# Performance work log

Measured on AMD Instinct MI355X. Metric: run time of the kernel, lower is better.

## Reference

```python
import jax, jax.numpy as jnp
import numpy as np

C = 128          # num_channels
HID = 256        # mlp hidden = 2*C
HEAD_DIM = 16    # C // num_heads (8)
SCALE = 1.0 / np.sqrt(HEAD_DIM)
EPS = 1e-5


def _linear_init(key, fan_in, fan_out):
    kw, kb = jax.random.split(key)
    s = 1.0 / np.sqrt(fan_in)
    w = jax.random.uniform(kw, (fan_in, fan_out), minval=-s, maxval=s, dtype=jnp.float32)
    b = jax.random.uniform(kb, (fan_out,), minval=-s, maxval=s, dtype=jnp.float32)
    return w, b


def setup_inputs() -> dict:
    key = jax.random.key(0)
    ks = jax.random.split(key, 8)
    x = jax.random.normal(ks[0], (4, C, 64, 64), dtype=jnp.float32)
    wq, bq = _linear_init(ks[1], C, C)
    wk, bk = _linear_init(ks[2], C, C)
    wv, bv = _linear_init(ks[3], C, C)
    wo, bo = _linear_init(ks[4], C, C)
    w1, b1 = _linear_init(ks[5], C, HID)
    w2, b2 = _linear_init(ks[6], HID, C)
    return {
        "x": x,
        "ln1_w": jnp.ones((C,), jnp.float32), "ln1_b": jnp.zeros((C,), jnp.float32),
        "wq": wq, "bq": bq, "wk": wk, "bk": bk, "wv": wv, "bv": bv,
        "wo": wo, "bo": bo,
        "ln2_w": jnp.ones((C,), jnp.float32), "ln2_b": jnp.zeros((C,), jnp.float32),
        "w1": w1, "b1": b1, "w2": w2, "b2": b2,
    }


def _layernorm(x, w, b):
    mu = jnp.mean(x, axis=-1, keepdims=True)
    var = jnp.mean(jnp.square(x - mu), axis=-1, keepdims=True)
    return (x - mu) * jax.lax.rsqrt(var + EPS) * w + b


def reference(x, ln1_w, ln1_b, wq, bq, wk, bk, wv, bv, wo, bo, ln2_w, ln2_b, w1, b1, w2, b2):
    B, Cc, H, W = x.shape
    t = x.reshape(B, Cc, H * W).transpose(0, 2, 1)  # [B, S, C]
    xl = _layernorm(t, ln1_w, ln1_b)
    q = xl @ wq + bq
    k = xl @ wk + bk
    v = xl @ wv + bv
    scores = jnp.einsum('bqc,bkc->bqk', q, k) * SCALE  # [B, S, S]
    # Faithful to source: softmax over dim=1 (the QUERY axis).
    attn = jax.nn.softmax(scores, axis=1)
    att_out = jnp.einsum('bqk,bkc->bqc', attn, v) @ wo + bo
    t = att_out + t
    m = _layernorm(t, ln2_w, ln2_b) @ w1 + b1
    m = jax.nn.gelu(m, approximate=False) @ w2 + b2
    t = jax.nn.gelu(m, approximate=False) + t  # second GELU per source
    return t.transpose(0, 2, 1).reshape(B, Cc, H, W)
```

## Files before the change

kernel.cpp:

```cpp
#include <hip/hip_runtime.h>
#include <math.h>

#define S 4096
#define CNUM 128
#define BATCH 4
#define MTOT (BATCH * S)
#define SCLOG2E 0.36067376022224085f
#define EPSLN 1e-5f
#define KSPLIT 8
#define QSPLIT 8


typedef __attribute__((ext_vector_type(8))) short bf16x8;
typedef __attribute__((ext_vector_type(4))) float f32x4;
typedef __attribute__((ext_vector_type(16))) float f32x16;
typedef __attribute__((ext_vector_type(4))) unsigned int u32x4;

__device__ __forceinline__ float gelu_exact(float x) {
    return 0.5f * x * (1.0f + erff(x * 0.7071067811865476f));
}

__device__ __forceinline__ unsigned short f2b(float f) {
    union { float f; unsigned int u; } v; v.f = f;
    unsigned int r = (v.u + 0x7FFFu + ((v.u >> 16) & 1u)) >> 16;
    return (unsigned short)r;
}
__device__ __forceinline__ float b2f(unsigned short u) {
    return __uint_as_float((unsigned)u << 16);
}
__device__ __forceinline__ int swz(int col, int row) {
    return ((((col >> 3) ^ (row & 15)) << 3) | (col & 7));
}

__device__ __forceinline__ void gl_lds16(const void* g, void* l) {
    __builtin_amdgcn_global_load_lds(
        (__attribute__((address_space(1))) void*)g,
        (__attribute__((address_space(3))) void*)l, 16, 0, 0);
}

__global__ __launch_bounds__(256) void ln1_transpose(
    const float* __restrict__ x, const float* __restrict__ w, const float* __restrict__ bb,
    unsigned short* __restrict__ xlh, float* __restrict__ t)
{
    __shared__ float tile[128][65];
    __shared__ float mu[64], rs[64];
    const int b = blockIdx.y;
    const int s0 = blockIdx.x * 64;
    const float* xb = x + (size_t)b * CNUM * S;
    for (int i = threadIdx.x; i < 128 * 64; i += 256) {
        int c = i >> 6, sl = i & 63;
        tile[c][sl] = xb[(size_t)c * S + s0 + sl];
    }
    __syncthreads();
    if (threadIdx.x < 64) {
        float sum = 0.f, sq = 0.f;
        for (int c = 0; c < 128; ++c) {
            float v = tile[c][threadIdx.x];
            sum += v; sq += v * v;
        }
        float m = sum * (1.f / 128.f);
        float var = sq * (1.f / 128.f) - m * m;
        mu[threadIdx.x] = m;
        rs[threadIdx.x] = rsqrtf(var + EPSLN);
    }
    __syncthreads();
    for (int i = threadIdx.x; i < 128 * 64; i += 256) {
        int c = i & 127, sl = i >> 7;
        float v = tile[c][sl];
        size_t row = (size_t)b * S + s0 + sl;
        t[row * CNUM + c] = v;
        xlh[row * CNUM + swz(c, sl)] = f2b((v - mu[sl]) * rs[sl] * w[c] + bb[c]);
    }
}

__global__ __launch_bounds__(256) void convw(
    const float* __restrict__ wq, const float* __restrict__ wk, const float* __restrict__ wv,
    const float* __restrict__ wo, const float* __restrict__ w1, const float* __restrict__ w2,
    const float* __restrict__ bq, const float* __restrict__ bk, const float* __restrict__ bv,
    unsigned short* __restrict__ wqkvh, unsigned short* __restrict__ woh,
    unsigned short* __restrict__ w1h, unsigned short* __restrict__ w2h,
    float* __restrict__ bqkv)
{
    int a = blockIdx.y;
    int idx = blockIdx.x * 256 + threadIdx.x;
    if (a == 6) {
        if (idx < 128) bqkv[idx] = bq[idx];
        else if (idx < 256) bqkv[idx] = bk[idx - 128];
        else if (idx < 384) bqkv[idx] = bv[idx - 256];
        return;
    }
    const float* src; unsigned short* dst; int Nsh, Ksz;
    switch (a) {
        case 0: src = wq; dst = wqkvh;          Nsh = 7; Ksz = 128; break;
        case 1: src = wk; dst = wqkvh + 16384;  Nsh = 7; Ksz = 128; break;
        case 2: src = wv; dst = wqkvh + 32768;  Nsh = 7; Ksz = 128; break;
        case 3: src = wo; dst = woh;            Nsh = 7; Ksz = 128; break;
        case 4: src = w1; dst = w1h;            Nsh = 8; Ksz = 128; break;
        default: src = w2; dst = w2h;           Nsh = 7; Ksz = 256; break;
    }
    int total = Ksz << Nsh;
    if (idx >= total) return;
    int k = idx >> Nsh, n = idx & ((1 << Nsh) - 1);
    dst[n * Ksz + swz(k, n)] = f2b(src[idx]);
}

template<int KT, int EPI>
__global__ __launch_bounds__(256) void gemm_mfma(
    const unsigned short* __restrict__ A, const unsigned short* __restrict__ Bt,
    const float* __restrict__ bias, const float* __restrict__ res,
    void* __restrict__ Cv, void* __restrict__ Cv2,
    const float* __restrict__ wln, const float* __restrict__ bln, int N)
{
    constexpr int CH = KT / 8;
    constexpr int CSH = (KT == 128) ? 4 : 5;
    __shared__ unsigned short As[64 * KT];
    __shared__ unsigned short Bs[128 * KT];
    __shared__ float2 lnred[2][64];
    const int bm = blockIdx.y * 64;
    const int bn = blockIdx.x * 128;
    const int z = blockIdx.z;
    const unsigned short* Btz = (EPI == 7) ? Bt + z * 16384 : Bt;
    const float* biasz = (EPI == 7) ? bias + z * 128 : bias;
    const int tid = threadIdx.x;
    const int w = tid >> 6, l = tid & 63;
    const int rw = (w & 1) * 32, cw = (w >> 1) * 64;
    const int lm = l & 15, lq = l >> 4;

    if (EPI == 3) {
        #pragma unroll
        for (int i = 0; i < (64 * CH) / 256; ++i) {
            int cid = i * 256 + tid;
            int r = cid >> CSH, c = cid & (CH - 1);
            int p = (c & ~15) | ((c ^ r) & 15);
            float s8[8];
            #pragma unroll
            for (int j = 0; j < 8; ++j) s8[j] = 0.f;
            #pragma unroll
            for (int pp = 0; pp < KSPLIT; ++pp) {
                const unsigned short* src = A + (size_t)pp * ((size_t)MTOT * CNUM)
                                              + (size_t)(bm + r) * KT + c * 8;
                ushort4 u0 = *(const ushort4*)(src);
                ushort4 u1 = *(const ushort4*)(src + 4);
                s8[0] += b2f(u0.x); s8[1] += b2f(u0.y); s8[2] += b2f(u0.z); s8[3] += b2f(u0.w);
                s8[4] += b2f(u1.x); s8[5] += b2f(u1.y); s8[6] += b2f(u1.z); s8[7] += b2f(u1.w);
            }
            ushort4 o0, o1;
            o0.x = f2b(s8[0]); o0.y = f2b(s8[1]); o0.z = f2b(s8[2]); o0.w = f2b(s8[3]);
            o1.x = f2b(s8[4]); o1.y = f2b(s8[5]); o1.z = f2b(s8[6]); o1.w = f2b(s8[7]);
            *(ushort4*)(As + r * KT + p * 8) = o0;
            *(ushort4*)(As + r * KT + p * 8 + 4) = o1;
        }
    } else {
        #pragma unroll
        for (int i = 0; i < KT / 32; ++i)
            gl_lds16(A + (size_t)bm * KT + (i * 256 + tid) * 8, As + (i * 256 + tid) * 8);
    }
    #pragma unroll
    for (int i = 0; i < KT / 16; ++i)
        gl_lds16(Btz + (size_t)bn * KT + (i * 256 + tid) * 8, Bs + (i * 256 + tid) * 8);
    __syncthreads();

    f32x4 zero = {0.f, 0.f, 0.f, 0.f};
    f32x4 acc[2][4];
    #pragma unroll
    for (int i = 0; i < 2; ++i)
        #pragma unroll
        for (int j = 0; j < 4; ++j) acc[i][j] = zero;

    #pragma unroll
    for (int ks = 0; ks < KT / 32; ++ks) {
        int c_lin = ks * 4 + lq;
        bf16x8 a[2], bfr[4];
        #pragma unroll
        for (int i = 0; i < 2; ++i) {
            int m = rw + i * 16 + lm;
            int p = (c_lin & ~15) | ((c_lin ^ m) & 15);
            a[i] = *(const bf16x8*)(As + m * KT + p * 8);
        }
        #pragma unroll
        for (int j = 0; j < 4; ++j) {
            int n = cw + j * 16 + lm;
            int p = (c_lin & ~15) | ((c_lin ^ n) & 15);
            bfr[j] = *(const bf16x8*)(Bs + n * KT + p * 8);
        }
        #pragma unroll
        for (int i = 0; i < 2; ++i)
            #pragma unroll
            for (int j = 0; j < 4; ++j)
                acc[i][j] = __builtin_amdgcn_mfma_f32_16x16x32_bf16(a[i], bfr[j], acc[i][j], 0, 0, 0);
    }

    if (EPI == 3) {
        float vv[2][4][4];
        #pragma unroll
        for (int i = 0; i < 2; ++i) {
            int rowbase = bm + rw + i * 16 + lq * 4;
            #pragma unroll
            for (int j = 0; j < 4; ++j) {
                int col = bn + cw + j * 16 + lm;
                #pragma unroll
                for (int reg = 0; reg < 4; ++reg)
                    vv[i][j][reg] = acc[i][j][reg] + biasz[col] +
                                    res[(size_t)(rowbase + reg) * N + col];
            }
        }
        #pragma unroll
        for (int i = 0; i < 2; ++i)
            #pragma unroll
            for (int reg = 0; reg < 4; ++reg) {
                float s = 0.f, q = 0.f;
                #pragma unroll
                for (int j = 0; j < 4; ++j) {
                    float xv = vv[i][j][reg];
                    s += xv; q += xv * xv;
                }
                #pragma unroll
                for (int off = 1; off < 16; off <<= 1) {
                    s += __shfl_xor(s, off);
                    q += __shfl_xor(q, off);
                }
                if (lm == 0) {
                    float2 sq2; sq2.x = s; sq2.y = q;
                    lnred[cw >> 6][rw + i * 16 + lq * 4 + reg] = sq2;
                }
            }
        __syncthreads();
        #pragma unroll
        for (int i = 0; i < 2; ++i) {
            #pragma unroll
            for (int reg = 0; reg < 4; ++reg) {
                int lrow = rw + i * 16 + lq * 4 + reg;
                int row = bm + lrow;
                float2 h0 = lnred[0][lrow], h1 = lnred[1][lrow];
                float mean = (h0.x + h1.x) * (1.f / 128.f);
                float var  = (h0.y + h1.y) * (1.f / 128.f) - mean * mean;
                float rs = rsqrtf(var + EPSLN);
                #pragma unroll
                for (int j = 0; j < 4; ++j) {
                    int col = bn + cw + j * 16 + lm;
                    float xv = vv[i][j][reg];
                    ((float*)Cv)[(size_t)row * N + col] = xv;
                    ((unsigned short*)Cv2)[(size_t)row * N + swz(col, lrow)] =
                        f2b((xv - mean) * rs * wln[col] + bln[col]);
                }
            }
        }
        return;
    }

    #pragma unroll
    for (int i = 0; i < 2; ++i) {
        int rowbase = bm + rw + i * 16 + lq * 4;
        #pragma unroll
        for (int j = 0; j < 4; ++j) {
            int col = bn + cw + j * 16 + lm;
            float v[4];
            #pragma unroll
            for (int reg = 0; reg < 4; ++reg) v[reg] = acc[i][j][reg] + biasz[col];
            if (EPI == 6) {
                #pragma unroll
                for (int reg = 0; reg < 4; ++reg)
                    ((unsigned short*)Cv)[(size_t)(rowbase + reg) * N + swz(col, rowbase + reg)] =
                        f2b(gelu_exact(v[reg]));
            } else if (EPI == 8) {
                int bb = rowbase >> 12, s = rowbase & 4095;
                float4 o;
                o.x = gelu_exact(v[0]) + res[(size_t)(rowbase + 0) * N + col];
                o.y = gelu_exact(v[1]) + res[(size_t)(rowbase + 1) * N + col];
                o.z = gelu_exact(v[2]) + res[(size_t)(rowbase + 2) * N + col];
                o.w = gelu_exact(v[3]) + res[(size_t)(rowbase + 3) * N + col];
                *(float4*)(((float*)Cv) + ((size_t)(bb * 128 + col)) * 4096 + s) = o;
            } else if (EPI == 7) {
                if (z < 2) {
                    unsigned short* dst = ((unsigned short*)Cv) + (size_t)z * MTOT * 128;
                    #pragma unroll
                    for (int reg = 0; reg < 4; ++reg)
                        dst[(size_t)(rowbase + reg) * 128 + swz(col, rowbase + reg)] = f2b(v[reg]);
                } else {
                    int bb = rowbase >> 12, s = rowbase & 4095;
                    int kc = s >> 6, g = (s >> 3) & 7;
                    ushort4 o;
                    o.x = f2b(v[0]); o.y = f2b(v[1]); o.z = f2b(v[2]); o.w = f2b(v[3]);
                    *(ushort4*)(((unsigned short*)Cv) + (size_t)2 * MTOT * 128 +
                                (((size_t)bb * 64 + kc) << 13) +
                                col * 64 + ((g ^ (col & 7)) << 3) + (s & 7)) = o;
                }
            }
        }
    }
}

__global__ __launch_bounds__(256) void colsum(
    const unsigned short* __restrict__ qh, const unsigned short* __restrict__ kh,
    float* __restrict__ psum_all)
{
    __shared__ unsigned short Qs[128 * 128];
    __shared__ unsigned short Ks[128 * 128];
    __shared__ float csum[2][128];
    const int b = blockIdx.z;
    const unsigned short* Q = qh + (size_t)b * S * 128;
    const unsigned short* Km = kh + (size_t)b * S * 128;
    const int bn = blockIdx.x * 128;
    const int q0 = blockIdx.y * (S / QSPLIT);
    const int tid = threadIdx.x;
    const int w = tid >> 6, l = tid & 63;
    const int wr = (w >> 1) * 64, wc = (w & 1) * 64;
    const int lm = l & 15, lq = l >> 4;

    #pragma unroll
    for (int i = 0; i < 8; ++i)
        gl_lds16(Km + (size_t)bn * 128 + (i * 256 + tid) * 8, Ks + (i * 256 + tid) * 8);

    float jsum[4] = {0.f, 0.f, 0.f, 0.f};
    for (int qt = 0; qt < (S / QSPLIT) / 128; ++qt) {
        __syncthreads();
        #pragma unroll
        for (int i = 0; i < 8; ++i)
            gl_lds16(Q + (size_t)(q0 + qt * 128) * 128 + (i * 256 + tid) * 8,
                     Qs + (i * 256 + tid) * 8);
        __syncthreads();

        f32x4 zero = {0.f, 0.f, 0.f, 0.f};
        f32x4 acc[4][4];
        #pragma unroll
        for (int i = 0; i < 4; ++i)
            #pragma unroll
            for (int j = 0; j < 4; ++j) acc[i][j] = zero;

        #pragma unroll
        for (int ks = 0; ks < 4; ++ks) {
            bf16x8 a[4], bfr[4];
            #pragma unroll
            for (int i = 0; i < 4; ++i) {
                int m = wr + i * 16 + lm;
                int p = (ks * 4 + lq) ^ (m & 15);
                a[i] = *(const bf16x8*)(Qs + m * 128 + p * 8);
            }
            #pragma unroll
            for (int j = 0; j < 4; ++j) {
                int n = wc + j * 16 + lm;
                int p = (ks * 4 + lq) ^ (n & 15);
                bfr[j] = *(const bf16x8*)(Ks + n * 128 + p * 8);
            }
            #pragma unroll
            for (int i = 0; i < 4; ++i)
                #pragma unroll
                for (int j = 0; j < 4; ++j)
                    acc[i][j] = __builtin_amdgcn_mfma_f32_16x16x32_bf16(a[i], bfr[j], acc[i][j], 0, 0, 0);
        }

        #pragma unroll
        for (int i = 0; i < 4; ++i)
            #pragma unroll
            for (int j = 0; j < 4; ++j)
                #pragma unroll
                for (int reg = 0; reg < 4; ++reg)
                    jsum[j] += exp2f(acc[i][j][reg] * SCLOG2E);
    }

    #pragma unroll
    for (int j = 0; j < 4; ++j) {
        jsum[j] += __shfl_xor(jsum[j], 16);
        jsum[j] += __shfl_xor(jsum[j], 32);
    }
    if (l < 16) {
        #pragma unroll
        for (int j = 0; j < 4; ++j)
            csum[w >> 1][wc + j * 16 + l] = jsum[j];
    }
    __syncthreads();
    if (tid < 128)
        psum_all[((size_t)(blockIdx.y * BATCH + b)) * S + bn + tid] = csum[0][tid] + csum[1][tid];
}

__global__ __launch_bounds__(256) void vscale(
    unsigned short* __restrict__ Vimg_all, const float* __restrict__ psum_all)
{
    const int b = blockIdx.z;
    unsigned short* Vimg = Vimg_all + (size_t)b * CNUM * S;
    int i = (blockIdx.x * 256 + threadIdx.x) * 4;
    int kc = i >> 13;
    int off = i & 8191;
    int c = off >> 6;
    int p = (off >> 3) & 7;
    int g = p ^ (c & 7);
    int k = kc * 64 + g * 8 + (off & 7);
    float4 L = *(const float4*)(psum_all + (size_t)b * S + k);
    #pragma unroll
    for (int t = 1; t < QSPLIT; ++t) {
        float4 Lt = *(const float4*)(psum_all + ((size_t)(t * BATCH + b)) * S + k);
        L.x += Lt.x; L.y += Lt.y; L.z += Lt.z; L.w += Lt.w;
    }
    ushort4 v = *(ushort4*)(Vimg + i);
    v.x = f2b(b2f(v.x) / L.x);
    v.y = f2b(b2f(v.y) / L.y);
    v.z = f2b(b2f(v.z) / L.z);
    v.w = f2b(b2f(v.w) / L.w);
    *(ushort4*)(Vimg + i) = v;
}

__global__ __launch_bounds__(256, 2) void fused_attnv(
    const unsigned short* __restrict__ qh, const unsigned short* __restrict__ kh,
    const unsigned short* __restrict__ Vimg_all, unsigned short* __restrict__ parts)
{
    __shared__ unsigned short Ks[32 * 128];
    __shared__ unsigned short Vls[128 * 64];
    const int b = blockIdx.z;
    const unsigned short* Qm = qh + (size_t)b * S * 128;
    const unsigned short* Km = kh + (size_t)b * S * 128;
    const unsigned short* Vimg = Vimg_all + (((size_t)b * 64) << 13);
    unsigned short* Pout = parts + (size_t)blockIdx.x * ((size_t)MTOT * CNUM)
                                 + (size_t)b * S * CNUM;
    const int q0 = blockIdx.y * 128;
    const int kb0 = blockIdx.x * (S / KSPLIT);
    const int kc0 = blockIdx.x * (S / KSPLIT / 64);
    const int tid = threadIdx.x;
    const int w = tid >> 6, l = tid & 63;
    const int lc = l & 31, lh = l >> 5;
    const int row0 = q0 + w * 32;

    bf16x8 aq[8];
    #pragma unroll
    for (int d = 0; d < 8; ++d)
        aq[d] = *(const bf16x8*)(Qm + (size_t)(row0 + lc) * 128 +
                                 (((d * 2 + lh) ^ (lc & 15)) << 3));

    f32x16 acco[4];
    #pragma unroll
    for (int cb = 0; cb < 4; ++cb)
        #pragma unroll
        for (int r = 0; r < 16; ++r) acco[cb][r] = 0.f;

    for (int kt = 0; kt < S / KSPLIT / 32; ++kt) {
        const int kb = kb0 + kt * 32;
        if (kt) __syncthreads();
        #pragma unroll
        for (int i2 = 0; i2 < 2; ++i2)
            gl_lds16(Km + (size_t)kb * 128 + (i2 * 256 + tid) * 8,
                     Ks + (i2 * 256 + tid) * 8);
        if ((kt & 1) == 0) {
            const unsigned short* src = Vimg + ((size_t)(kc0 + (kt >> 1)) << 13) + tid * 8;
            #pragma unroll
            for (int i2 = 0; i2 < 4; ++i2)
                gl_lds16(src + i2 * 2048, &Vls[(i2 * 256 + tid) * 8]);
        }
        __syncthreads();

        f32x16 accT;
        #pragma unroll
        for (int r = 0; r < 16; ++r) accT[r] = 0.f;
        #pragma unroll
        for (int d = 0; d < 8; ++d) {
            int slot = d * 2 + lh;
            bf16x8 kf = *(const bf16x8*)(Ks + lc * 128 + ((slot ^ (lc & 15)) << 3));
            accT = __builtin_amdgcn_mfma_f32_32x32x16_bf16(kf, aq[d], accT, 0, 0, 0);
        }

        unsigned int pk[4][2];
        #pragma unroll
        for (int t = 0; t < 4; ++t)
            #pragma unroll
            for (int p = 0; p < 2; ++p) {
                float e0 = exp2f(accT[t * 4 + 2 * p]     * SCLOG2E);
                float e1 = exp2f(accT[t * 4 + 2 * p + 1] * SCLOG2E);
                asm("v_cvt_pk_bf16_f32 %0, %1, %2" : "=v"(pk[t][p]) : "v"(e0), "v"(e1));
            }
        #pragma unroll
        for (int p = 0; p < 2; ++p) {
            asm volatile("v_permlane32_swap_b32 %0, %1" : "+v"(pk[0][p]), "+v"(pk[1][p]));
            asm volatile("v_permlane32_swap_b32 %0, %1" : "+v"(pk[2][p]), "+v"(pk[3][p]));
        }
        u32x4 u0 = {pk[0][0], pk[0][1], pk[1][0], pk[1][1]};
        u32x4 u1 = {pk[2][0], pk[2][1], pk[3][0], pk[3][1]};
        bf16x8 ap0 = __builtin_bit_cast(bf16x8, u0);
        bf16x8 ap1 = __builtin_bit_cast(bf16x8, u1);

        const int g0 = (kt & 1) * 4 + lh;
        const int g1 = g0 + 2;
        __builtin_amdgcn_s_setprio(1);
        #pragma unroll
        for (int cb = 0; cb < 4; ++cb) {
            int c = cb * 32 + lc;
            bf16x8 v0 = *(const bf16x8*)(Vls + c * 64 + ((g0 ^ (c & 7)) << 3));
            bf16x8 v1 = *(const bf16x8*)(Vls + c * 64 + ((g1 ^ (c & 7)) << 3));
            acco[cb] = __builtin_amdgcn_mfma_f32_32x32x16_bf16(ap0, v0, acco[cb], 0, 0, 0);
            acco[cb] = __builtin_amdgcn_mfma_f32_32x32x16_bf16(ap1, v1, acco[cb], 0, 0, 0);
        }
        __builtin_amdgcn_s_setprio(0);
    }

    #pragma unroll
    for (int cb = 0; cb < 4; ++cb)
        #pragma unroll
        for (int r = 0; r < 16; ++r) {
            int q = (r & 3) + 8 * (r >> 2) + 4 * lh;
            Pout[(size_t)(row0 + q) * CNUM + cb * 32 + lc] = f2b(acco[cb][r]);
        }
}

extern "C" void kernel_launch(void* const* d_in, const int* in_sizes, int n_in,
                              void* d_out, int out_size, void* d_ws, size_t ws_size,
                              hipStream_t stream)
{
    (void)in_sizes; (void)n_in; (void)out_size; (void)ws_size;
    const float* x    = (const float*)d_in[0];
    const float* ln1w = (const float*)d_in[1];
    const float* ln1b = (const float*)d_in[2];
    const float* wq   = (const float*)d_in[3];
    const float* bq   = (const float*)d_in[4];
    const float* wk   = (const float*)d_in[5];
    const float* bk   = (const float*)d_in[6];
    const float* wv   = (const float*)d_in[7];
    const float* bv   = (const float*)d_in[8];
    const float* wo   = (const float*)d_in[9];
    const float* bo   = (const float*)d_in[10];
    const float* ln2w = (const float*)d_in[11];
    const float* ln2b = (const float*)d_in[12];
    const float* w1   = (const float*)d_in[13];
    const float* b1   = (const float*)d_in[14];
    const float* w2   = (const float*)d_in[15];
    const float* b2   = (const float*)d_in[16];
    float* out = (float*)d_out;

    float* ws = (float*)d_ws;
    const size_t NSC = (size_t)MTOT * CNUM;
    float* t      = ws;
    float* y      = t + NSC;
    float* psum   = y + NSC;
    unsigned short* parts = (unsigned short*)(psum + (size_t)QSPLIT * BATCH * S);
    unsigned short* xlh = parts + (size_t)KSPLIT * NSC;
    unsigned short* qh  = xlh + NSC;
    unsigned short* kh  = qh + NSC;
    unsigned short* Vt  = kh + NSC;
    unsigned short* zh  = Vt + NSC;
    unsigned short* hh  = zh + NSC;
    unsigned short* wqkvh = hh + (size_t)MTOT * 256;
    unsigned short* woh = wqkvh + 3 * 16384;
    unsigned short* w1h = woh + 16384;
    unsigned short* w2h = w1h + 32768;
    float* bqkv = (float*)(w2h + 32768);

    ln1_transpose<<<dim3(S / 64, BATCH), 256, 0, stream>>>(x, ln1w, ln1b, xlh, t);
    convw<<<dim3(128, 7), 256, 0, stream>>>(wq, wk, wv, wo, w1, w2, bq, bk, bv,
                                            wqkvh, woh, w1h, w2h, bqkv);

    gemm_mfma<128, 7><<<dim3(1, MTOT / 64, 3), 256, 0, stream>>>(
        xlh, wqkvh, bqkv, nullptr, qh, nullptr, nullptr, nullptr, 128);

    colsum<<<dim3(S / 128, QSPLIT, BATCH), 256, 0, stream>>>(qh, kh, psum);
    vscale<<<dim3(CNUM * S / 4 / 256, 1, BATCH), 256, 0, stream>>>(Vt, psum);
    fused_attnv<<<dim3(KSPLIT, S / 128, BATCH), 256, 0, stream>>>(qh, kh, Vt, parts);

    gemm_mfma<128, 3><<<dim3(1, MTOT / 64), 256, 0, stream>>>(
        parts, woh, bo, t, y, zh, ln2w, ln2b, 128);
    gemm_mfma<128, 6><<<dim3(2, MTOT / 64), 256, 0, stream>>>(
        zh, w1h, b1, nullptr, hh, nullptr, nullptr, nullptr, 256);
    gemm_mfma<256, 8><<<dim3(1, MTOT / 64), 256, 0, stream>>>(
        hh, w2h, b2, y, out, nullptr, nullptr, nullptr, 128);
}
```

Baseline: 229.1 us.

## Triple-buffer K and double-buffer V in fused attention; fold softmax scale into Q

The fused attention-V kernel now prefetches the next K tile into a 3-slot LDS ring and the next V chunk into a 2-slot buffer. Explicit vmcnt waits and a single barrier per iteration replace the two syncthreads around synchronous loads. This is meant to overlap global-to-LDS traffic with the MFMA work. Separately, the softmax scale times log2(e) is folded into Q in the QKV projection epilogue, removing a multiply per score in colsum and fused_attnv, at the cost of slightly different bf16 rounding of Q and more LDS per block, which may lower occupancy.

```diff
diff --git a/kernel.cpp b/kernel.cpp
--- a/kernel.cpp
+++ b/kernel.cpp
@@ -274,8 +274,10 @@
                 if (z < 2) {
                     unsigned short* dst = ((unsigned short*)Cv) + (size_t)z * MTOT * 128;
                     #pragma unroll
-                    for (int reg = 0; reg < 4; ++reg)
-                        dst[(size_t)(rowbase + reg) * 128 + swz(col, rowbase + reg)] = f2b(v[reg]);
+                    for (int reg = 0; reg < 4; ++reg) {
+                        float ov = (z == 0) ? v[reg] * SCLOG2E : v[reg];
+                        dst[(size_t)(rowbase + reg) * 128 + swz(col, rowbase + reg)] = f2b(ov);
+                    }
                 } else {
                     int bb = rowbase >> 12, s = rowbase & 4095;
                     int kc = s >> 6, g = (s >> 3) & 7;
@@ -355,7 +357,7 @@
             for (int j = 0; j < 4; ++j)
                 #pragma unroll
                 for (int reg = 0; reg < 4; ++reg)
-                    jsum[j] += exp2f(acc[i][j][reg] * SCLOG2E);
+                    jsum[j] += exp2f(acc[i][j][reg]);
     }
 
     #pragma unroll
@@ -403,8 +405,8 @@
     const unsigned short* __restrict__ qh, const unsigned short* __restrict__ kh,
     const unsigned short* __restrict__ Vimg_all, unsigned short* __restrict__ parts)
 {
-    __shared__ unsigned short Ks[32 * 128];
-    __shared__ unsigned short Vls[128 * 64];
+    __shared__ unsigned short Ks[3][32 * 128];
+    __shared__ unsigned short Vls[2][128 * 64];
     const int b = blockIdx.z;
     const unsigned short* Qm = qh + (size_t)b * S * 128;
     const unsigned short* Km = kh + (size_t)b * S * 128;
@@ -431,20 +433,39 @@
         #pragma unroll
         for (int r = 0; r < 16; ++r) acco[cb][r] = 0.f;
 
-    for (int kt = 0; kt < S / KSPLIT / 32; ++kt) {
-        const int kb = kb0 + kt * 32;
-        if (kt) __syncthreads();
-        #pragma unroll
-        for (int i2 = 0; i2 < 2; ++i2)
-            gl_lds16(Km + (size_t)kb * 128 + (i2 * 256 + tid) * 8,
-                     Ks + (i2 * 256 + tid) * 8);
-        if ((kt & 1) == 0) {
-            const unsigned short* src = Vimg + ((size_t)(kc0 + (kt >> 1)) << 13) + tid * 8;
+    {
+        const unsigned short* ksrc = Km + (size_t)kb0 * 128 + tid * 8;
+        gl_lds16(ksrc,        &Ks[0][tid * 8]);
+        gl_lds16(ksrc + 2048, &Ks[0][(256 + tid) * 8]);
+        const unsigned short* vsrc = Vimg + ((size_t)kc0 << 13) + tid * 8;
+        #pragma unroll
+        for (int i2 = 0; i2 < 4; ++i2)
+            gl_lds16(vsrc + i2 * 2048, &Vls[0][(i2 * 256 + tid) * 8]);
+    }
+
+    int kcur = 0;
+    for (int kt = 0; kt < 16; ++kt) {
+        int knx = kcur + 1; if (knx == 3) knx = 0;
+        if (kt < 15) {
+            const unsigned short* ksrc = Km + (size_t)(kb0 + (kt + 1) * 32) * 128 + tid * 8;
+            gl_lds16(ksrc,        &Ks[knx][tid * 8]);
+            gl_lds16(ksrc + 2048, &Ks[knx][(256 + tid) * 8]);
+        }
+        if ((kt & 1) == 0)      asm volatile("s_waitcnt vmcnt(2)" ::: "memory");
+        else if (kt < 15)       asm volatile("s_waitcnt vmcnt(6)" ::: "memory");
+        else                    asm volatile("s_waitcnt vmcnt(0)" ::: "memory");
+        __builtin_amdgcn_s_barrier();
+        if ((kt & 1) == 0 && (kt >> 1) + 1 < 8) {
+            int vn = (kt >> 1) + 1;
+            const unsigned short* vsrc = Vimg + ((size_t)(kc0 + vn) << 13) + tid * 8;
+            unsigned short* vdst = Vls[vn & 1];
             #pragma unroll
             for (int i2 = 0; i2 < 4; ++i2)
-                gl_lds16(src + i2 * 2048, &Vls[(i2 * 256 + tid) * 8]);
-        }
-        __syncthreads();
+                gl_lds16(vsrc + i2 * 2048, vdst + (i2 * 256 + tid) * 8);
+        }
+
+        const unsigned short* Kbuf = Ks[kcur];
+        const unsigned short* Vbuf = Vls[(kt >> 1) & 1];
 
         f32x16 accT;
         #pragma unroll
@@ -452,7 +473,7 @@
         #pragma unroll
         for (int d = 0; d < 8; ++d) {
             int slot = d * 2 + lh;
-            bf16x8 kf = *(const bf16x8*)(Ks + lc * 128 + ((slot ^ (lc & 15)) << 3));
+            bf16x8 kf = *(const bf16x8*)(Kbuf + lc * 128 + ((slot ^ (lc & 15)) << 3));
             accT = __builtin_amdgcn_mfma_f32_32x32x16_bf16(kf, aq[d], accT, 0, 0, 0);
         }
 
@@ -461,8 +482,8 @@
         for (int t = 0; t < 4; ++t)
             #pragma unroll
             for (int p = 0; p < 2; ++p) {
-                float e0 = exp2f(accT[t * 4 + 2 * p]     * SCLOG2E);
-                float e1 = exp2f(accT[t * 4 + 2 * p + 1] * SCLOG2E);
+                float e0 = exp2f(accT[t * 4 + 2 * p]);
+                float e1 = exp2f(accT[t * 4 + 2 * p + 1]);
                 asm("v_cvt_pk_bf16_f32 %0, %1, %2" : "=v"(pk[t][p]) : "v"(e0), "v"(e1));
             }
         #pragma unroll
@@ -481,12 +502,13 @@
         #pragma unroll
         for (int cb = 0; cb < 4; ++cb) {
             int c = cb * 32 + lc;
-            bf16x8 v0 = *(const bf16x8*)(Vls + c * 64 + ((g0 ^ (c & 7)) << 3));
-            bf16x8 v1 = *(const bf16x8*)(Vls + c * 64 + ((g1 ^ (c & 7)) << 3));
+            bf16x8 v0 = *(const bf16x8*)(Vbuf + c * 64 + ((g0 ^ (c & 7)) << 3));
+            bf16x8 v1 = *(const bf16x8*)(Vbuf + c * 64 + ((g1 ^ (c & 7)) << 3));
             acco[cb] = __builtin_amdgcn_mfma_f32_32x32x16_bf16(ap0, v0, acco[cb], 0, 0, 0);
             acco[cb] = __builtin_amdgcn_mfma_f32_32x32x16_bf16(ap1, v1, acco[cb], 0, 0, 0);
         }
         __builtin_amdgcn_s_setprio(0);
+        kcur = knx;
     }
 
     #pragma unroll
```

Result: no change. 226.9 us (-1.0%).

## Halve GEMM row tile, split K=256 B staging, fold softmax scale into Q

Applied to the files above, without the earlier changes.

The GEMM kernel gains a BM template parameter. All four projection/MLP GEMMs switch to 32-row tiles, with each warp owning a 32-column strip, which doubles the block count and reduces per-block LDS. For K=256 the B tile is now staged in two 128-wide phases to shrink shared memory, and the LayerNorm reduction is generalized to four column groups. The softmax scale*log2e is folded into the Q projection output, so the exp2 in colsum and fused_attnv drops a multiply, at the cost of an extra bf16 rounding on the scaled Q values.

```diff
diff --git a/kernel.cpp b/kernel.cpp
--- a/kernel.cpp
+++ b/kernel.cpp
@@ -104,7 +104,7 @@
     dst[n * Ksz + swz(k, n)] = f2b(src[idx]);
 }
 
-template<int KT, int EPI>
+template<int KT, int EPI, int BM>
 __global__ __launch_bounds__(256) void gemm_mfma(
     const unsigned short* __restrict__ A, const unsigned short* __restrict__ Bt,
     const float* __restrict__ bias, const float* __restrict__ res,
@@ -113,90 +113,108 @@
 {
     constexpr int CH = KT / 8;
     constexpr int CSH = (KT == 128) ? 4 : 5;
-    __shared__ unsigned short As[64 * KT];
-    __shared__ unsigned short Bs[128 * KT];
-    __shared__ float2 lnred[2][64];
-    const int bm = blockIdx.y * 64;
+    constexpr int BKT = (KT == 256) ? 128 : KT;
+    constexpr int NPH = KT / BKT;
+    constexpr int NJ = (BM == 64) ? 4 : 2;
+    constexpr int NG = 128 / (NJ * 16);
+    __shared__ unsigned short As[BM * KT];
+    __shared__ unsigned short Bs[128 * BKT];
+    __shared__ float2 lnred[(EPI == 3) ? NG * BM : 1];
+    const int bm = blockIdx.y * BM;
     const int bn = blockIdx.x * 128;
     const int z = blockIdx.z;
     const unsigned short* Btz = (EPI == 7) ? Bt + z * 16384 : Bt;
     const float* biasz = (EPI == 7) ? bias + z * 128 : bias;
     const int tid = threadIdx.x;
     const int w = tid >> 6, l = tid & 63;
-    const int rw = (w & 1) * 32, cw = (w >> 1) * 64;
+    const int rw = (BM == 64) ? (w & 1) * 32 : 0;
+    const int cw = (BM == 64) ? (w >> 1) * 64 : w * 32;
     const int lm = l & 15, lq = l >> 4;
 
+    f32x4 zero = {0.f, 0.f, 0.f, 0.f};
+    f32x4 acc[2][NJ];
+    #pragma unroll
+    for (int i = 0; i < 2; ++i)
+        #pragma unroll
+        for (int j = 0; j < NJ; ++j) acc[i][j] = zero;
+
+    #pragma unroll
+    for (int ph = 0; ph < NPH; ++ph) {
+        if (ph == 0) {
+            if (EPI == 3) {
+                #pragma unroll
+                for (int i = 0; i < (BM * CH) / 256; ++i) {
+                    int cid = i * 256 + tid;
+                    int r = cid >> CSH, c = cid & (CH - 1);
+                    int p = (c & ~15) | ((c ^ r) & 15);
+                    float s8[8];
+                    #pragma unroll
+                    for (int j = 0; j < 8; ++j) s8[j] = 0.f;
+                    #pragma unroll
+                    for (int pp = 0; pp < KSPLIT; ++pp) {
+                        const unsigned short* src = A + (size_t)pp * ((size_t)MTOT * CNUM)
+                                                      + (size_t)(bm + r) * KT + c * 8;
+                        ushort4 u0 = *(const ushort4*)(src);
+                        ushort4 u1 = *(const ushort4*)(src + 4);
+                        s8[0] += b2f(u0.x); s8[1] += b2f(u0.y); s8[2] += b2f(u0.z); s8[3] += b2f(u0.w);
+                        s8[4] += b2f(u1.x); s8[5] += b2f(u1.y); s8[6] += b2f(u1.z); s8[7] += b2f(u1.w);
+                    }
+                    ushort4 o0, o1;
+                    o0.x = f2b(s8[0]); o0.y = f2b(s8[1]); o0.z = f2b(s8[2]); o0.w = f2b(s8[3]);
+                    o1.x = f2b(s8[4]); o1.y = f2b(s8[5]); o1.z = f2b(s8[6]); o1.w = f2b(s8[7]);
+                    *(ushort4*)(As + r * KT + p * 8) = o0;
+                    *(ushort4*)(As + r * KT + p * 8 + 4) = o1;
+                }
+            } else {
+                #pragma unroll
+                for (int i = 0; i < (BM * CH) / 256; ++i)
+                    gl_lds16(A + (size_t)bm * KT + (i * 256 + tid) * 8,
+                             As + (i * 256 + tid) * 8);
+            }
+        } else {
+            __syncthreads();
+        }
+        #pragma unroll
+        for (int i = 0; i < (128 * BKT / 8) / 256; ++i) {
+            int cid = i * 256 + tid;
+            int n = cid >> (CSH - (NPH - 1)), gg = cid & (BKT / 8 - 1);
+            gl_lds16(Btz + (size_t)(bn + n) * KT + ph * BKT + gg * 8,
+                     Bs + cid * 8);
+        }
+        __syncthreads();
+
+        #pragma unroll
+        for (int ks = 0; ks < BKT / 32; ++ks) {
+            int c_loc = ks * 4 + lq;
+            int c_glob = ph * 16 + c_loc;
+            bf16x8 a[2], bfr[NJ];
+            #pragma unroll
+            for (int i = 0; i < 2; ++i) {
+                int m = rw + i * 16 + lm;
+                int p = (c_glob & ~15) | ((c_glob ^ m) & 15);
+                a[i] = *(const bf16x8*)(As + m * KT + p * 8);
+            }
+            #pragma unroll
+            for (int j = 0; j < NJ; ++j) {
+                int n = cw + j * 16 + lm;
+                int p = (c_loc ^ n) & 15;
+                bfr[j] = *(const bf16x8*)(Bs + n * BKT + p * 8);
+            }
+            #pragma unroll
+            for (int i = 0; i < 2; ++i)
+                #pragma unroll
+                for (int j = 0; j < NJ; ++j)
+                    acc[i][j] = __builtin_amdgcn_mfma_f32_16x16x32_bf16(a[i], bfr[j], acc[i][j], 0, 0, 0);
+        }
+    }
+
     if (EPI == 3) {
-        #pragma unroll
-        for (int i = 0; i < (64 * CH) / 256; ++i) {
-            int cid = i * 256 + tid;
-            int r = cid >> CSH, c = cid & (CH - 1);
-            int p = (c & ~15) | ((c ^ r) & 15);
-            float s8[8];
-            #pragma unroll
-            for (int j = 0; j < 8; ++j) s8[j] = 0.f;
-            #pragma unroll
-            for (int pp = 0; pp < KSPLIT; ++pp) {
-                const unsigned short* src = A + (size_t)pp * ((size_t)MTOT * CNUM)
-                                              + (size_t)(bm + r) * KT + c * 8;
-                ushort4 u0 = *(const ushort4*)(src);
-                ushort4 u1 = *(const ushort4*)(src + 4);
-                s8[0] += b2f(u0.x); s8[1] += b2f(u0.y); s8[2] += b2f(u0.z); s8[3] += b2f(u0.w);
-                s8[4] += b2f(u1.x); s8[5] += b2f(u1.y); s8[6] += b2f(u1.z); s8[7] += b2f(u1.w);
-            }
-            ushort4 o0, o1;
-            o0.x = f2b(s8[0]); o0.y = f2b(s8[1]); o0.z = f2b(s8[2]); o0.w = f2b(s8[3]);
-            o1.x = f2b(s8[4]); o1.y = f2b(s8[5]); o1.z = f2b(s8[6]); o1.w = f2b(s8[7]);
-            *(ushort4*)(As + r * KT + p * 8) = o0;
-            *(ushort4*)(As + r * KT + p * 8 + 4) = o1;
-        }
-    } else {
-        #pragma unroll
-        for (int i = 0; i < KT / 32; ++i)
-            gl_lds16(A + (size_t)bm * KT + (i * 256 + tid) * 8, As + (i * 256 + tid) * 8);
-    }
-    #pragma unroll
-    for (int i = 0; i < KT / 16; ++i)
-        gl_lds16(Btz + (size_t)bn * KT + (i * 256 + tid) * 8, Bs + (i * 256 + tid) * 8);
-    __syncthreads();
-
-    f32x4 zero = {0.f, 0.f, 0.f, 0.f};
-    f32x4 acc[2][4];
-    #pragma unroll
-    for (int i = 0; i < 2; ++i)
-        #pragma unroll
-        for (int j = 0; j < 4; ++j) acc[i][j] = zero;
-
-    #pragma unroll
-    for (int ks = 0; ks < KT / 32; ++ks) {
-        int c_lin = ks * 4 + lq;
-        bf16x8 a[2], bfr[4];
-        #pragma unroll
-        for (int i = 0; i < 2; ++i) {
-            int m = rw + i * 16 + lm;
-            int p = (c_lin & ~15) | ((c_lin ^ m) & 15);
-            a[i] = *(const bf16x8*)(As + m * KT + p * 8);
-        }
-        #pragma unroll
-        for (int j = 0; j < 4; ++j) {
-            int n = cw + j * 16 + lm;
-            int p = (c_lin & ~15) | ((c_lin ^ n) & 15);
-            bfr[j] = *(const bf16x8*)(Bs + n * KT + p * 8);
-        }
-        #pragma unroll
-        for (int i = 0; i < 2; ++i)
-            #pragma unroll
-            for (int j = 0; j < 4; ++j)
-                acc[i][j] = __builtin_amdgcn_mfma_f32_16x16x32_bf16(a[i], bfr[j], acc[i][j], 0, 0, 0);
-    }
-
-    if (EPI == 3) {
-        float vv[2][4][4];
+        float vv[2][NJ][4];
         #pragma unroll
         for (int i = 0; i < 2; ++i) {
             int rowbase = bm + rw + i * 16 + lq * 4;
             #pragma unroll
-            for (int j = 0; j < 4; ++j) {
+            for (int j = 0; j < NJ; ++j) {
                 int col = bn + cw + j * 16 + lm;
                 #pragma unroll
                 for (int reg = 0; reg < 4; ++reg)
@@ -210,7 +228,7 @@
             for (int reg = 0; reg < 4; ++reg) {
                 float s = 0.f, q = 0.f;
                 #pragma unroll
-                for (int j = 0; j < 4; ++j) {
+                for (int j = 0; j < NJ; ++j) {
                     float xv = vv[i][j][reg];
                     s += xv; q += xv * xv;
                 }
@@ -221,7 +239,7 @@
                 }
                 if (lm == 0) {
                     float2 sq2; sq2.x = s; sq2.y = q;
-                    lnred[cw >> 6][rw + i * 16 + lq * 4 + reg] = sq2;
+                    lnred[(cw / (NJ * 16)) * BM + rw + i * 16 + lq * 4 + reg] = sq2;
                 }
             }
         __syncthreads();
@@ -231,12 +249,17 @@
             for (int reg = 0; reg < 4; ++reg) {
                 int lrow = rw + i * 16 + lq * 4 + reg;
                 int row = bm + lrow;
-                float2 h0 = lnred[0][lrow], h1 = lnred[1][lrow];
-                float mean = (h0.x + h1.x) * (1.f / 128.f);
-                float var  = (h0.y + h1.y) * (1.f / 128.f) - mean * mean;
+                float sx = 0.f, sq = 0.f;
+                #pragma unroll
+                for (int g = 0; g < NG; ++g) {
+                    float2 h = lnred[g * BM + lrow];
+                    sx += h.x; sq += h.y;
+                }
+                float mean = sx * (1.f / 128.f);
+                float var  = sq * (1.f / 128.f) - mean * mean;
                 float rs = rsqrtf(var + EPSLN);
                 #pragma unroll
-                for (int j = 0; j < 4; ++j) {
+                for (int j = 0; j < NJ; ++j) {
                     int col = bn + cw + j * 16 + lm;
                     float xv = vv[i][j][reg];
                     ((float*)Cv)[(size_t)row * N + col] = xv;
@@ -252,7 +275,7 @@
     for (int i = 0; i < 2; ++i) {
         int rowbase = bm + rw + i * 16 + lq * 4;
         #pragma unroll
-        for (int j = 0; j < 4; ++j) {
+        for (int j = 0; j < NJ; ++j) {
             int col = bn + cw + j * 16 + lm;
             float v[4];
             #pragma unroll
@@ -274,8 +297,10 @@
                 if (z < 2) {
                     unsigned short* dst = ((unsigned short*)Cv) + (size_t)z * MTOT * 128;
                     #pragma unroll
-                    for (int reg = 0; reg < 4; ++reg)
-                        dst[(size_t)(rowbase + reg) * 128 + swz(col, rowbase + reg)] = f2b(v[reg]);
+                    for (int reg = 0; reg < 4; ++reg) {
+                        float ov = (z == 0) ? v[reg] * SCLOG2E : v[reg];
+                        dst[(size_t)(rowbase + reg) * 128 + swz(col, rowbase + reg)] = f2b(ov);
+                    }
                 } else {
                     int bb = rowbase >> 12, s = rowbase & 4095;
                     int kc = s >> 6, g = (s >> 3) & 7;
@@ -355,7 +380,7 @@
             for (int j = 0; j < 4; ++j)
                 #pragma unroll
                 for (int reg = 0; reg < 4; ++reg)
-                    jsum[j] += exp2f(acc[i][j][reg] * SCLOG2E);
+                    jsum[j] += exp2f(acc[i][j][reg]);
     }
 
     #pragma unroll
@@ -461,8 +486,8 @@
         for (int t = 0; t < 4; ++t)
             #pragma unroll
             for (int p = 0; p < 2; ++p) {
-                float e0 = exp2f(accT[t * 4 + 2 * p]     * SCLOG2E);
-                float e1 = exp2f(accT[t * 4 + 2 * p + 1] * SCLOG2E);
+                float e0 = exp2f(accT[t * 4 + 2 * p]);
+                float e1 = exp2f(accT[t * 4 + 2 * p + 1]);
                 asm("v_cvt_pk_bf16_f32 %0, %1, %2" : "=v"(pk[t][p]) : "v"(e0), "v"(e1));
             }
         #pragma unroll
@@ -544,17 +569,17 @@
     convw<<<dim3(128, 7), 256, 0, stream>>>(wq, wk, wv, wo, w1, w2, bq, bk, bv,
                                             wqkvh, woh, w1h, w2h, bqkv);
 
-    gemm_mfma<128, 7><<<dim3(1, MTOT / 64, 3), 256, 0, stream>>>(
+    gemm_mfma<128, 7, 32><<<dim3(1, MTOT / 32, 3), 256, 0, stream>>>(
         xlh, wqkvh, bqkv, nullptr, qh, nullptr, nullptr, nullptr, 128);
 
     colsum<<<dim3(S / 128, QSPLIT, BATCH), 256, 0, stream>>>(qh, kh, psum);
     vscale<<<dim3(CNUM * S / 4 / 256, 1, BATCH), 256, 0, stream>>>(Vt, psum);
     fused_attnv<<<dim3(KSPLIT, S / 128, BATCH), 256, 0, stream>>>(qh, kh, Vt, parts);
 
-    gemm_mfma<128, 3><<<dim3(1, MTOT / 64), 256, 0, stream>>>(
+    gemm_mfma<128, 3, 32><<<dim3(1, MTOT / 32), 256, 0, stream>>>(
         parts, woh, bo, t, y, zh, ln2w, ln2b, 128);
-    gemm_mfma<128, 6><<<dim3(2, MTOT / 64), 256, 0, stream>>>(
+    gemm_mfma<128, 6, 32><<<dim3(2, MTOT / 32), 256, 0, stream>>>(
         zh, w1h, b1, nullptr, hh, nullptr, nullptr, nullptr, 256);
-    gemm_mfma<256, 8><<<dim3(1, MTOT / 64), 256, 0, stream>>>(
+    gemm_mfma<256, 8, 32><<<dim3(1, MTOT / 32), 256, 0, stream>>>(
         hh, w2h, b2, y, out, nullptr, nullptr, nullptr, 128);
 }
```

New measurement: 224.0 us. 2.2% less time.
